# Kernel optimization log

Measured on AMD Instinct MI355X. Metric: run time of the kernel, lower is better.

## Reference

```python
import jax, jax.numpy as jnp
import numpy as np

B, I, S = 1024, 128, 512
UNFOLDS = 6


def setup_inputs() -> dict:
    key = jax.random.key(0)
    ks = jax.random.split(key, 16)
    inputs = jax.random.normal(ks[0], (B, I), dtype=jnp.float32)
    hx = jax.random.normal(ks[1], (B, S), dtype=jnp.float32)
    # learned parameters, initialized per _get_variables()
    input_w = jnp.ones((I,), dtype=jnp.float32)
    input_b = jnp.zeros((I,), dtype=jnp.float32)
    sensory_mu = jax.random.uniform(ks[2], (I, S)) * 0.5 + 0.3
    sensory_sigma = jax.random.uniform(ks[3], (I, S)) * 5.0 + 3.0
    sensory_W = jax.random.uniform(ks[4], (I, S), minval=0.01, maxval=1.0)
    sensory_erev = (2.0 * jax.random.randint(ks[5], (I, S), 0, 2) - 1.0).astype(jnp.float32)
    mu = jax.random.uniform(ks[6], (S, S)) * 0.5 + 0.3
    sigma = jax.random.uniform(ks[7], (S, S)) * 5.0 + 3.0
    W = jax.random.uniform(ks[8], (S, S), minval=0.01, maxval=1.0)
    erev = (2.0 * jax.random.randint(ks[9], (S, S), 0, 2) - 1.0).astype(jnp.float32)
    vleak = jax.random.uniform(ks[10], (S,)) * 0.4 - 0.2
    gleak = jnp.ones((S,), dtype=jnp.float32)   # gleak_init_min == gleak_init_max == 1
    cm_t = jnp.full((S,), 0.5, dtype=jnp.float32)  # cm_init_min == cm_init_max == 0.5
    return dict(inputs=inputs, hx=hx, input_w=input_w, input_b=input_b,
                sensory_mu=sensory_mu, sensory_sigma=sensory_sigma,
                sensory_W=sensory_W, sensory_erev=sensory_erev,
                mu=mu, sigma=sigma, W=W, erev=erev,
                vleak=vleak, gleak=gleak, cm_t=cm_t)


def reference(inputs, hx, input_w, input_b, sensory_mu, sensory_sigma,
              sensory_W, sensory_erev, mu, sigma, W, erev, vleak, gleak, cm_t):
    # Affine input mapping
    x = inputs * input_w + input_b                      # [B, I]
    # Sensory synapse activation (computed once): [B, I, S]
    sens_act = sensory_W * jax.nn.sigmoid(sensory_sigma * (x[:, :, None] - sensory_mu))
    w_num_sensory = jnp.sum(sens_act * sensory_erev, axis=1)  # [B, S]
    w_den_sensory = jnp.sum(sens_act, axis=1)                 # [B, S]

    v = hx
    for _ in range(UNFOLDS):
        # Recurrent synapse activation: broadcast state over presynaptic dim -> [B, S, S]
        w_act = W * jax.nn.sigmoid(sigma * (v[:, :, None] - mu))
        w_num = jnp.sum(w_act * erev, axis=1) + w_num_sensory   # [B, S]
        w_den = jnp.sum(w_act, axis=1) + w_den_sensory          # [B, S]
        numerator = cm_t * v + gleak * vleak + w_num
        denominator = cm_t + gleak + w_den
        v = numerator / denominator
    # forward returns (outputs, next_state), which are the same tensor
    return v
```

## Files before the change

kernel.cpp:

```cpp
#include <hip/hip_runtime.h>
#include <hip/hip_bf16.h>
#include <math.h>


#define B_TOT 1024
#define I_DIM 128
#define S_DIM 512
#define UNFOLDS 6
#define BT 4
#define TBL_N 4096
#define T_MAX 14.0f

__global__ __launch_bounds__(256) void prep_kernel(
    const float* __restrict__ sens_mu, const float* __restrict__ sens_sigma,
    const float* __restrict__ sens_W, const float* __restrict__ sens_erev,
    const float* __restrict__ mu, const float* __restrict__ sigma,
    const float* __restrict__ W, const float* __restrict__ erev,
    float4* __restrict__ recP, float4* __restrict__ sensP)
{
    const float L2E   = 1.4426950408889634f;
    const float SCALE = (float)TBL_N / (2.0f * T_MAX);
    const float OFF   = (float)(TBL_N / 2) + 0.5f;
    int idx = blockIdx.x * 256 + threadIdx.x;
    if (idx < I_DIM * S_DIM) {
        float sg = sens_sigma[idx], m = sens_mu[idx], w = sens_W[idx], er = sens_erev[idx];
        float A = -sg * L2E, C = sg * m * L2E;
        sensP[idx] = make_float4(A * SCALE, C * SCALE + OFF, w * er, w);
    }
    if (idx < S_DIM * S_DIM) {
        float sg = sigma[idx], m = mu[idx], w = W[idx], er = erev[idx];
        float A = -sg * L2E, C = sg * m * L2E;
        recP[idx] = make_float4(A * SCALE, C * SCALE + OFF, w * er, w);
    }
}

__global__ __launch_bounds__(512, 2) void liquid_main(
    const float* __restrict__ inputs,
    const float* __restrict__ hx,
    const float* __restrict__ input_w,
    const float* __restrict__ input_b,
    const float4* __restrict__ sensP,
    const float4* __restrict__ recP,
    const float* __restrict__ vleak,
    const float* __restrict__ gleak,
    const float* __restrict__ cm_t,
    float* __restrict__ out)
{
    const int j = threadIdx.x;
    const int b0 = blockIdx.x * BT;

    __shared__ float tbl[TBL_N];
    __shared__ float xs[BT][I_DIM];
    __shared__ float vs[BT][S_DIM];

    {
        const float INV_SCALE = (2.0f * T_MAX) / (float)TBL_N;
        for (int k = threadIdx.x; k < TBL_N; k += S_DIM) {
            float tc = ((float)k - (float)(TBL_N / 2)) * INV_SCALE;
            tbl[k] = 1.0f / (1.0f + exp2f(tc));
        }
    }

    {
        int b = threadIdx.x >> 7, ii = threadIdx.x & 127;
        xs[b][ii] = inputs[(b0 + b) * I_DIM + ii] * input_w[ii] + input_b[ii];
    }
    #pragma unroll
    for (int k = 0; k < BT; ++k)
        vs[k][j] = hx[(b0 + k) * S_DIM + j];
    __syncthreads();

    const float CLHI = (float)(TBL_N - 1);

    float snum[BT], sden[BT];
    #pragma unroll
    for (int b = 0; b < BT; ++b) { snum[b] = 0.f; sden[b] = 0.f; }

    for (int i = 0; i < I_DIM; i += 4) {
        float4 p[4];
        #pragma unroll
        for (int u = 0; u < 4; ++u) p[u] = sensP[(i + u) * S_DIM + j];
        #pragma unroll
        for (int b = 0; b < BT; ++b) {
            float4 xv4 = *(const float4*)&xs[b][i];
            float xv[4] = {xv4.x, xv4.y, xv4.z, xv4.w};
            #pragma unroll
            for (int u = 0; u < 4; ++u) {
                float f = fmaf(p[u].x, xv[u], p[u].y);
                f = __builtin_amdgcn_fmed3f(f, 0.0f, CLHI);
                float s = tbl[(unsigned)f];
                snum[b] = fmaf(p[u].z, s, snum[b]);
                sden[b] = fmaf(p[u].w, s, sden[b]);
            }
        }
    }

    const float gl = gleak[j], vl = vleak[j], cmj = cm_t[j];
    const float glvl = gl * vl;
    const float cg = cmj + gl;

    for (int it = 0; it < UNFOLDS; ++it) {
        float num[BT], den[BT];
        #pragma unroll
        for (int b = 0; b < BT; ++b) { num[b] = snum[b]; den[b] = sden[b]; }

        for (int i = 0; i < S_DIM; i += 4) {
            float4 p[4];
            #pragma unroll
            for (int u = 0; u < 4; ++u) p[u] = recP[(i + u) * S_DIM + j];
            #pragma unroll
            for (int b = 0; b < BT; ++b) {
                float4 vv4 = *(const float4*)&vs[b][i];
                float vv[4] = {vv4.x, vv4.y, vv4.z, vv4.w};
                #pragma unroll
                for (int u = 0; u < 4; ++u) {
                    float f = fmaf(p[u].x, vv[u], p[u].y);
                    f = __builtin_amdgcn_fmed3f(f, 0.0f, CLHI);
                    float s = tbl[(unsigned)f];
                    num[b] = fmaf(p[u].z, s, num[b]);
                    den[b] = fmaf(p[u].w, s, den[b]);
                }
            }
        }

        float vnew[BT];
        #pragma unroll
        for (int b = 0; b < BT; ++b) {
            float vold = vs[b][j];
            vnew[b] = (fmaf(cmj, vold, glvl) + num[b]) / (cg + den[b]);
        }
        __syncthreads();
        #pragma unroll
        for (int b = 0; b < BT; ++b) vs[b][j] = vnew[b];
        __syncthreads();
    }

    #pragma unroll
    for (int b = 0; b < BT; ++b)
        out[(b0 + b) * S_DIM + j] = vs[b][j];
}

extern "C" void kernel_launch(void* const* d_in, const int* in_sizes, int n_in,
                              void* d_out, int out_size, void* d_ws, size_t ws_size,
                              hipStream_t stream) {
    const float* inputs   = (const float*)d_in[0];
    const float* hx       = (const float*)d_in[1];
    const float* input_w  = (const float*)d_in[2];
    const float* input_b  = (const float*)d_in[3];
    const float* s_mu     = (const float*)d_in[4];
    const float* s_sigma  = (const float*)d_in[5];
    const float* s_W      = (const float*)d_in[6];
    const float* s_erev   = (const float*)d_in[7];
    const float* mu       = (const float*)d_in[8];
    const float* sigma    = (const float*)d_in[9];
    const float* W        = (const float*)d_in[10];
    const float* erev     = (const float*)d_in[11];
    const float* vleak    = (const float*)d_in[12];
    const float* gleak    = (const float*)d_in[13];
    const float* cm_t     = (const float*)d_in[14];
    float* out = (float*)d_out;

    float4* recP  = (float4*)d_ws;
    float4* sensP = (float4*)((char*)d_ws + (size_t)S_DIM * S_DIM * sizeof(float4));

    int prep_threads = S_DIM * S_DIM;
    prep_kernel<<<(prep_threads + 255) / 256, 256, 0, stream>>>(
        s_mu, s_sigma, s_W, s_erev, mu, sigma, W, erev, recP, sensP);

    liquid_main<<<B_TOT / BT, S_DIM, 0, stream>>>(
        inputs, hx, input_w, input_b, sensP, recP, vleak, gleak, cm_t, out);
}
```

Before: 423.7 us.

## Restructure into per-neuron unfold kernels with exp2 sigmoid and transposed state

Replaces the single fused kernel with several kernels. A prep kernel transposes the parameters, inputs and state into column-major workspace arrays. A sensory kernel runs once, and then one kernel per unfold step, each block owning one postsynaptic neuron and its threads spanning the batch. The shared-memory sigmoid lookup table is replaced by a hardware exp2 plus a bit-trick reciprocal refined with two Newton steps. Per-neuron parameters now become uniform scalar loads and the state is ping-ponged through global memory. This aims to remove LDS table gathers and bank conflicts, at the cost of extra kernel launches, global round-trips of the state, and more ALU work per sigmoid.

```diff
diff --git a/kernel.cpp b/kernel.cpp
--- a/kernel.cpp
+++ b/kernel.cpp
@@ -1,5 +1,4 @@
 #include <hip/hip_runtime.h>
-#include <hip/hip_bf16.h>
 #include <math.h>
 
 
@@ -7,137 +6,177 @@
 #define I_DIM 128
 #define S_DIM 512
 #define UNFOLDS 6
-#define BT 4
-#define TBL_N 4096
-#define T_MAX 14.0f
-
-__global__ __launch_bounds__(256) void prep_kernel(
-    const float* __restrict__ sens_mu, const float* __restrict__ sens_sigma,
-    const float* __restrict__ sens_W, const float* __restrict__ sens_erev,
+#define L2E 1.4426950408889634f
+
+#define OFF_RECA 0
+#define OFF_RECC (OFF_RECA + S_DIM * S_DIM)
+#define OFF_RECW (OFF_RECC + S_DIM * S_DIM)
+#define OFF_SENA (OFF_RECW + S_DIM * S_DIM)
+#define OFF_SENC (OFF_SENA + S_DIM * I_DIM)
+#define OFF_SENW (OFF_SENC + S_DIM * I_DIM)
+#define OFF_XT   (OFF_SENW + S_DIM * I_DIM)
+#define OFF_VA   (OFF_XT + I_DIM * B_TOT)
+#define OFF_VB   (OFF_VA + S_DIM * B_TOT)
+#define OFF_SN   (OFF_VB + S_DIM * B_TOT)
+#define OFF_SD   (OFF_SN + S_DIM * B_TOT)
+
+__device__ __forceinline__ float rcp_nr2(float d) {
+    float y = __int_as_float(0x7EF311C3 - __float_as_int(d));
+    y = y * fmaf(-d, y, 2.0f);
+    y = y * fmaf(-d, y, 2.0f);
+    return y;
+}
+
+__device__ __forceinline__ float sigv(float a, float c, float v) {
+    float t = fmaf(a, v, c);
+    t = __builtin_amdgcn_fmed3f(t, -126.0f, 126.0f);
+    float e = __builtin_amdgcn_exp2f(t);
+    return rcp_nr2(1.0f + e);
+}
+
+__global__ __launch_bounds__(256) void prep_all(
+    const float* __restrict__ inputs, const float* __restrict__ hx,
+    const float* __restrict__ input_w, const float* __restrict__ input_b,
+    const float* __restrict__ s_mu, const float* __restrict__ s_sigma,
+    const float* __restrict__ s_W, const float* __restrict__ s_erev,
     const float* __restrict__ mu, const float* __restrict__ sigma,
     const float* __restrict__ W, const float* __restrict__ erev,
-    float4* __restrict__ recP, float4* __restrict__ sensP)
-{
-    const float L2E   = 1.4426950408889634f;
-    const float SCALE = (float)TBL_N / (2.0f * T_MAX);
-    const float OFF   = (float)(TBL_N / 2) + 0.5f;
-    int idx = blockIdx.x * 256 + threadIdx.x;
-    if (idx < I_DIM * S_DIM) {
-        float sg = sens_sigma[idx], m = sens_mu[idx], w = sens_W[idx], er = sens_erev[idx];
-        float A = -sg * L2E, C = sg * m * L2E;
-        sensP[idx] = make_float4(A * SCALE, C * SCALE + OFF, w * er, w);
-    }
-    if (idx < S_DIM * S_DIM) {
-        float sg = sigma[idx], m = mu[idx], w = W[idx], er = erev[idx];
-        float A = -sg * L2E, C = sg * m * L2E;
-        recP[idx] = make_float4(A * SCALE, C * SCALE + OFF, w * er, w);
-    }
-}
-
-__global__ __launch_bounds__(512, 2) void liquid_main(
-    const float* __restrict__ inputs,
-    const float* __restrict__ hx,
-    const float* __restrict__ input_w,
-    const float* __restrict__ input_b,
-    const float4* __restrict__ sensP,
-    const float4* __restrict__ recP,
-    const float* __restrict__ vleak,
-    const float* __restrict__ gleak,
+    float* __restrict__ ws)
+{
+    __shared__ float tA[32][33], tB[32][33], tC[32][33];
+    const int bid = blockIdx.x;
+    const int tx = threadIdx.x & 31, ty = threadIdx.x >> 5;
+
+    if (bid < 320) {
+        bool rec = bid < 256;
+        int b2  = rec ? bid : bid - 256;
+        int tri = b2 >> 4;
+        int tcj = b2 & 15;
+        const float* sgp = rec ? sigma : s_sigma;
+        const float* mup = rec ? mu    : s_mu;
+        const float* wp  = rec ? W     : s_W;
+        const float* erp = rec ? erev  : s_erev;
+        #pragma unroll
+        for (int rr = 0; rr < 4; ++rr) {
+            int r = ty + rr * 8;
+            int idx = (tri * 32 + r) * S_DIM + tcj * 32 + tx;
+            float sg = sgp[idx], m = mup[idx], w = wp[idx], er = erp[idx];
+            tA[r][tx] = -sg * L2E;
+            tB[r][tx] = sg * m * L2E;
+            tC[r][tx] = w * er;
+        }
+        __syncthreads();
+        float* dA = ws + (rec ? OFF_RECA : OFF_SENA);
+        float* dC = ws + (rec ? OFF_RECC : OFF_SENC);
+        float* dW = ws + (rec ? OFF_RECW : OFF_SENW);
+        int ld = rec ? S_DIM : I_DIM;
+        #pragma unroll
+        for (int rr = 0; rr < 4; ++rr) {
+            int jj = ty + rr * 8;
+            int o = (tcj * 32 + jj) * ld + tri * 32 + tx;
+            dA[o] = tA[tx][jj];
+            dC[o] = tB[tx][jj];
+            dW[o] = tC[tx][jj];
+        }
+    } else if (bid < 448) {
+        int b2 = bid - 320;
+        int tbr = b2 >> 2;
+        int tci = b2 & 3;
+        int i = tci * 32 + tx;
+        float wi = input_w[i], bi = input_b[i];
+        #pragma unroll
+        for (int rr = 0; rr < 4; ++rr) {
+            int r = ty + rr * 8;
+            tA[r][tx] = inputs[(tbr * 32 + r) * I_DIM + i] * wi + bi;
+        }
+        __syncthreads();
+        float* xT = ws + OFF_XT;
+        #pragma unroll
+        for (int rr = 0; rr < 4; ++rr) {
+            int ii = ty + rr * 8;
+            xT[(tci * 32 + ii) * B_TOT + tbr * 32 + tx] = tA[tx][ii];
+        }
+    } else {
+        int b2 = bid - 448;
+        int tbr = b2 >> 4;
+        int tcj = b2 & 15;
+        #pragma unroll
+        for (int rr = 0; rr < 4; ++rr) {
+            int r = ty + rr * 8;
+            tA[r][tx] = hx[(tbr * 32 + r) * S_DIM + tcj * 32 + tx];
+        }
+        __syncthreads();
+        float* vA = ws + OFF_VA;
+        #pragma unroll
+        for (int rr = 0; rr < 4; ++rr) {
+            int jj = ty + rr * 8;
+            vA[(tcj * 32 + jj) * B_TOT + tbr * 32 + tx] = tA[tx][jj];
+        }
+    }
+}
+
+__device__ __forceinline__ void col_reduce(
+    const float* __restrict__ pA, const float* __restrict__ pC,
+    const float* __restrict__ pW, const float* __restrict__ vsrc,
+    int nd, int tb, float& n0, float& n1, float& d0, float& d1)
+{
+    #pragma unroll 8
+    for (int i = 0; i < nd; ++i) {
+        float a = pA[i], c = pC[i], w = pW[i];
+        const float* p = vsrc + i * B_TOT;
+        float2 v = *(const float2*)&p[tb];
+        float s0 = sigv(a, c, v.x);
+        float s1 = sigv(a, c, v.y);
+        n0 = fmaf(w, s0, n0);
+        d0 = fmaf(fabsf(w), s0, d0);
+        n1 = fmaf(w, s1, n1);
+        d1 = fmaf(fabsf(w), s1, d1);
+    }
+}
+
+__global__ __launch_bounds__(512, 4) void sensory_kernel(float* __restrict__ ws)
+{
+    const int j = blockIdx.x;
+    const int tb = threadIdx.x * 2;
+    const float* pA = ws + OFF_SENA + j * I_DIM;
+    const float* pC = ws + OFF_SENC + j * I_DIM;
+    const float* pW = ws + OFF_SENW + j * I_DIM;
+    float n0 = 0.f, n1 = 0.f, d0 = 0.f, d1 = 0.f;
+    col_reduce(pA, pC, pW, ws + OFF_XT, I_DIM, tb, n0, n1, d0, d1);
+    *(float2*)&ws[OFF_SN + j * B_TOT + tb] = make_float2(n0, n1);
+    *(float2*)&ws[OFF_SD + j * B_TOT + tb] = make_float2(d0, d1);
+}
+
+__global__ __launch_bounds__(512, 4) void unfold_kernel(
+    const float* __restrict__ ws, const float* __restrict__ vsrc,
+    float* __restrict__ vdst,
+    const float* __restrict__ gleak, const float* __restrict__ vleak,
     const float* __restrict__ cm_t,
-    float* __restrict__ out)
-{
-    const int j = threadIdx.x;
-    const int b0 = blockIdx.x * BT;
-
-    __shared__ float tbl[TBL_N];
-    __shared__ float xs[BT][I_DIM];
-    __shared__ float vs[BT][S_DIM];
-
-    {
-        const float INV_SCALE = (2.0f * T_MAX) / (float)TBL_N;
-        for (int k = threadIdx.x; k < TBL_N; k += S_DIM) {
-            float tc = ((float)k - (float)(TBL_N / 2)) * INV_SCALE;
-            tbl[k] = 1.0f / (1.0f + exp2f(tc));
-        }
-    }
-
-    {
-        int b = threadIdx.x >> 7, ii = threadIdx.x & 127;
-        xs[b][ii] = inputs[(b0 + b) * I_DIM + ii] * input_w[ii] + input_b[ii];
-    }
-    #pragma unroll
-    for (int k = 0; k < BT; ++k)
-        vs[k][j] = hx[(b0 + k) * S_DIM + j];
-    __syncthreads();
-
-    const float CLHI = (float)(TBL_N - 1);
-
-    float snum[BT], sden[BT];
-    #pragma unroll
-    for (int b = 0; b < BT; ++b) { snum[b] = 0.f; sden[b] = 0.f; }
-
-    for (int i = 0; i < I_DIM; i += 4) {
-        float4 p[4];
-        #pragma unroll
-        for (int u = 0; u < 4; ++u) p[u] = sensP[(i + u) * S_DIM + j];
-        #pragma unroll
-        for (int b = 0; b < BT; ++b) {
-            float4 xv4 = *(const float4*)&xs[b][i];
-            float xv[4] = {xv4.x, xv4.y, xv4.z, xv4.w};
-            #pragma unroll
-            for (int u = 0; u < 4; ++u) {
-                float f = fmaf(p[u].x, xv[u], p[u].y);
-                f = __builtin_amdgcn_fmed3f(f, 0.0f, CLHI);
-                float s = tbl[(unsigned)f];
-                snum[b] = fmaf(p[u].z, s, snum[b]);
-                sden[b] = fmaf(p[u].w, s, sden[b]);
-            }
-        }
-    }
-
-    const float gl = gleak[j], vl = vleak[j], cmj = cm_t[j];
-    const float glvl = gl * vl;
-    const float cg = cmj + gl;
-
-    for (int it = 0; it < UNFOLDS; ++it) {
-        float num[BT], den[BT];
-        #pragma unroll
-        for (int b = 0; b < BT; ++b) { num[b] = snum[b]; den[b] = sden[b]; }
-
-        for (int i = 0; i < S_DIM; i += 4) {
-            float4 p[4];
-            #pragma unroll
-            for (int u = 0; u < 4; ++u) p[u] = recP[(i + u) * S_DIM + j];
-            #pragma unroll
-            for (int b = 0; b < BT; ++b) {
-                float4 vv4 = *(const float4*)&vs[b][i];
-                float vv[4] = {vv4.x, vv4.y, vv4.z, vv4.w};
-                #pragma unroll
-                for (int u = 0; u < 4; ++u) {
-                    float f = fmaf(p[u].x, vv[u], p[u].y);
-                    f = __builtin_amdgcn_fmed3f(f, 0.0f, CLHI);
-                    float s = tbl[(unsigned)f];
-                    num[b] = fmaf(p[u].z, s, num[b]);
-                    den[b] = fmaf(p[u].w, s, den[b]);
-                }
-            }
-        }
-
-        float vnew[BT];
-        #pragma unroll
-        for (int b = 0; b < BT; ++b) {
-            float vold = vs[b][j];
-            vnew[b] = (fmaf(cmj, vold, glvl) + num[b]) / (cg + den[b]);
-        }
-        __syncthreads();
-        #pragma unroll
-        for (int b = 0; b < BT; ++b) vs[b][j] = vnew[b];
-        __syncthreads();
-    }
-
-    #pragma unroll
-    for (int b = 0; b < BT; ++b)
-        out[(b0 + b) * S_DIM + j] = vs[b][j];
+    float* __restrict__ out, int write_out)
+{
+    const int j = blockIdx.x;
+    const int tb = threadIdx.x * 2;
+    const float* pA = ws + OFF_RECA + j * S_DIM;
+    const float* pC = ws + OFF_RECC + j * S_DIM;
+    const float* pW = ws + OFF_RECW + j * S_DIM;
+    float n0 = 0.f, n1 = 0.f, d0 = 0.f, d1 = 0.f;
+    col_reduce(pA, pC, pW, vsrc, S_DIM, tb, n0, n1, d0, d1);
+
+    float2 sn = *(const float2*)&ws[OFF_SN + j * B_TOT + tb];
+    float2 sd = *(const float2*)&ws[OFF_SD + j * B_TOT + tb];
+    float2 vo = *(const float2*)&vsrc[j * B_TOT + tb];
+    float gl = gleak[j], vl = vleak[j], cm = cm_t[j];
+    float glvl = gl * vl, cg = cm + gl;
+
+    float r0 = (fmaf(cm, vo.x, glvl) + n0 + sn.x) / (cg + d0 + sd.x);
+    float r1 = (fmaf(cm, vo.y, glvl) + n1 + sn.y) / (cg + d1 + sd.y);
+
+    if (write_out) {
+        out[tb * S_DIM + j] = r0;
+        out[(tb + 1) * S_DIM + j] = r1;
+    } else {
+        *(float2*)&vdst[j * B_TOT + tb] = make_float2(r0, r1);
+    }
 }
 
 extern "C" void kernel_launch(void* const* d_in, const int* in_sizes, int n_in,
@@ -159,14 +198,21 @@
     const float* gleak    = (const float*)d_in[13];
     const float* cm_t     = (const float*)d_in[14];
     float* out = (float*)d_out;
-
-    float4* recP  = (float4*)d_ws;
-    float4* sensP = (float4*)((char*)d_ws + (size_t)S_DIM * S_DIM * sizeof(float4));
-
-    int prep_threads = S_DIM * S_DIM;
-    prep_kernel<<<(prep_threads + 255) / 256, 256, 0, stream>>>(
-        s_mu, s_sigma, s_W, s_erev, mu, sigma, W, erev, recP, sensP);
-
-    liquid_main<<<B_TOT / BT, S_DIM, 0, stream>>>(
-        inputs, hx, input_w, input_b, sensP, recP, vleak, gleak, cm_t, out);
-}
+    float* ws  = (float*)d_ws;
+
+    prep_all<<<960, 256, 0, stream>>>(inputs, hx, input_w, input_b,
+                                      s_mu, s_sigma, s_W, s_erev,
+                                      mu, sigma, W, erev, ws);
+
+    sensory_kernel<<<S_DIM, 512, 0, stream>>>(ws);
+
+    float* vA = ws + OFF_VA;
+    float* vB = ws + OFF_VB;
+    for (int u = 0; u < UNFOLDS; ++u) {
+        const float* src = (u & 1) ? vB : vA;
+        float* dst       = (u & 1) ? vA : vB;
+        int last = (u == UNFOLDS - 1);
+        unfold_kernel<<<S_DIM, 512, 0, stream>>>(
+            ws, src, dst, gleak, vleak, cm_t, out, last);
+    }
+}
```

After: 523.8 us. 1.24x slower.
